# Performance work log

Measured on AMD Instinct MI355X. Metric: run time of the kernel, lower is better.

## Reference

```python
import jax, jax.numpy as jnp
import numpy as np

N_NODES = 50000
N_EDGES = 1250000
H_FEATS = 64


def setup_inputs() -> dict:
    key = jax.random.key(0)
    k1, k2, k3, k4, k5, k6, k7 = jax.random.split(key, 7)
    h = jax.random.normal(k1, (N_NODES, H_FEATS), dtype=jnp.float32)
    src = jax.random.randint(k2, (N_EDGES,), 0, N_NODES, dtype=jnp.int64)
    dst = jax.random.randint(k3, (N_EDGES,), 0, N_NODES, dtype=jnp.int64)
    # nn.Linear(2*h, h) and nn.Linear(h, 1); store weights as [in, out]
    s1 = 1.0 / np.sqrt(2 * H_FEATS)
    s2 = 1.0 / np.sqrt(H_FEATS)
    W1 = jax.random.uniform(k4, (2 * H_FEATS, H_FEATS), jnp.float32, -s1, s1)
    b1 = jax.random.uniform(k5, (H_FEATS,), jnp.float32, -s1, s1)
    W2 = jax.random.uniform(k6, (H_FEATS, 1), jnp.float32, -s2, s2)
    b2 = jax.random.uniform(k7, (1,), jnp.float32, -s2, s2)
    return {"h": h, "src": src, "dst": dst, "W1": W1, "b1": b1, "W2": W2, "b2": b2}


def reference(h, src, dst, W1, b1, W2, b2):
    # Gather per-edge endpoint features and concat: [E, 2*h_feats]
    he = jnp.concatenate([h[src], h[dst]], axis=1)
    hid = jax.nn.relu(he @ W1 + b1)          # [E, h_feats]
    score = (hid @ W2 + b2)[:, 0]            # [E]
    label = jnp.round(jax.nn.sigmoid(score))  # [E]
    return score, label
```

## Files before the change

### kernel.cpp

```cpp
#include <hip/hip_runtime.h>
#include <hip/hip_bf16.h>

#define H 64
#define NPB 64
#define EPB 128

__global__ void __launch_bounds__(256)
node_proj_kernel(const float* __restrict__ h,
                 const float* __restrict__ W1,
                 float* __restrict__ A,
                 float* __restrict__ B,
                 int n_nodes) {
    __shared__ float sh[NPB * H];
    const int t = threadIdx.x;
    const int c = t & 63;
    const int w = t >> 6;
    const int base = blockIdx.x * NPB;

    {
        const float4* hg = (const float4*)(h + (size_t)base * H);
        float4* shv = (float4*)sh;
#pragma unroll
        for (int i = 0; i < 4; ++i) {
            const int idx = t + i * 256;
            const int node = base + (idx >> 4);
            if (node < n_nodes) shv[idx] = hg[idx];
        }
    }

    float wA[64], wB[64];
#pragma unroll
    for (int k = 0; k < 64; ++k) {
        wA[k] = W1[k * H + c];
        wB[k] = W1[(k + 64) * H + c];
    }
    __syncthreads();

#pragma unroll 1
    for (int n0 = 0; n0 < 8; ++n0) {
        const int nl = w * 16 + n0 * 2;
        const int node = base + nl;
        if (node >= n_nodes) break;
        const bool two = (node + 1) < n_nodes;
        const float4* hr0 = (const float4*)(sh + nl * H);
        const float4* hr1 = (const float4*)(sh + (nl + 1) * H);
        float a0 = 0.f, b0 = 0.f, a1 = 0.f, b1acc = 0.f;
#pragma unroll
        for (int kk = 0; kk < 16; ++kk) {
            const float4 h0 = hr0[kk];
            const float4 h1 = hr1[kk];
            a0 = fmaf(h0.x, wA[4 * kk + 0], a0);
            a0 = fmaf(h0.y, wA[4 * kk + 1], a0);
            a0 = fmaf(h0.z, wA[4 * kk + 2], a0);
            a0 = fmaf(h0.w, wA[4 * kk + 3], a0);
            b0 = fmaf(h0.x, wB[4 * kk + 0], b0);
            b0 = fmaf(h0.y, wB[4 * kk + 1], b0);
            b0 = fmaf(h0.z, wB[4 * kk + 2], b0);
            b0 = fmaf(h0.w, wB[4 * kk + 3], b0);
            a1 = fmaf(h1.x, wA[4 * kk + 0], a1);
            a1 = fmaf(h1.y, wA[4 * kk + 1], a1);
            a1 = fmaf(h1.z, wA[4 * kk + 2], a1);
            a1 = fmaf(h1.w, wA[4 * kk + 3], a1);
            b1acc = fmaf(h1.x, wB[4 * kk + 0], b1acc);
            b1acc = fmaf(h1.y, wB[4 * kk + 1], b1acc);
            b1acc = fmaf(h1.z, wB[4 * kk + 2], b1acc);
            b1acc = fmaf(h1.w, wB[4 * kk + 3], b1acc);
        }
        A[(size_t)node * H + c] = a0;
        B[(size_t)node * H + c] = b0;
        if (two) {
            A[(size_t)(node + 1) * H + c] = a1;
            B[(size_t)(node + 1) * H + c] = b1acc;
        }
    }
}

__global__ void __launch_bounds__(256)
edge_score_kernel(const float* __restrict__ A,
                  const float* __restrict__ B,
                  const int* __restrict__ src,
                  const int* __restrict__ dst,
                  const float* __restrict__ b1,
                  const float* __restrict__ W2,
                  const float* __restrict__ b2,
                  float* __restrict__ score_out,
                  float* __restrict__ label_out,
                  int n_edges) {
    const int t = threadIdx.x;
    const int sub = t & 15;
    const int group = t >> 4;

    const float4 b1v = ((const float4*)b1)[sub];
    const float4 w2v = ((const float4*)W2)[sub];
    const float b2s = b2[0];

    const int e0 = blockIdx.x * EPB + group;

    int ec[8], s[8], d[8];
#pragma unroll
    for (int i = 0; i < 8; ++i) {
        const int e = e0 + i * 16;
        ec[i] = e < n_edges ? e : (n_edges - 1);
    }
#pragma unroll
    for (int i = 0; i < 8; ++i) { s[i] = src[ec[i]]; d[i] = dst[ec[i]]; }

    float4 a4[8], c4[8];
#pragma unroll
    for (int i = 0; i < 8; ++i)
        a4[i] = ((const float4*)(A + (size_t)s[i] * H))[sub];
#pragma unroll
    for (int i = 0; i < 8; ++i)
        c4[i] = ((const float4*)(B + (size_t)d[i] * H))[sub];

#pragma unroll
    for (int i = 0; i < 8; ++i) {
        const float h0 = fmaxf(a4[i].x + c4[i].x + b1v.x, 0.f);
        const float h1 = fmaxf(a4[i].y + c4[i].y + b1v.y, 0.f);
        const float h2 = fmaxf(a4[i].z + c4[i].z + b1v.z, 0.f);
        const float h3 = fmaxf(a4[i].w + c4[i].w + b1v.w, 0.f);
        float p = h0 * w2v.x + h1 * w2v.y + h2 * w2v.z + h3 * w2v.w;
        p += __shfl_xor(p, 1);
        p += __shfl_xor(p, 2);
        p += __shfl_xor(p, 4);
        p += __shfl_xor(p, 8);
        const int e = e0 + i * 16;
        if (sub == 0 && e < n_edges) {
            const float sc = p + b2s;
            score_out[e] = sc;
            label_out[e] = sc > 0.f ? 1.f : 0.f;
        }
    }
}

extern "C" void kernel_launch(void* const* d_in, const int* in_sizes, int n_in,
                              void* d_out, int out_size, void* d_ws, size_t ws_size,
                              hipStream_t stream) {
    const float* h   = (const float*)d_in[0];
    const int*   src = (const int*)  d_in[1];
    const int*   dst = (const int*)  d_in[2];
    const float* W1  = (const float*)d_in[3];
    const float* b1  = (const float*)d_in[4];
    const float* W2  = (const float*)d_in[5];
    const float* b2  = (const float*)d_in[6];

    const int n_nodes = in_sizes[0] / H;
    const int n_edges = in_sizes[1];

    float* A = (float*)d_ws;
    float* B = A + (size_t)n_nodes * H;

    float* score_out = (float*)d_out;
    float* label_out = score_out + n_edges;

    {
        const int blocks = (n_nodes + NPB - 1) / NPB;
        node_proj_kernel<<<blocks, 256, 0, stream>>>(h, W1, A, B, n_nodes);
    }
    {
        const int blocks = (n_edges + EPB - 1) / EPB;
        edge_score_kernel<<<blocks, 256, 0, stream>>>(A, B, src, dst, b1, W2, b2,
                                                      score_out, label_out, n_edges);
    }
}
```

Measured before the change: 172.7 us.

## Gather bf16 node projections in edge kernel with fp32 fallback near zero

The node projection kernel now writes both fp32 and bf16 copies of the A/B projections. The edge kernel gathers the half-size bf16 rows to cut random-gather traffic. When the resulting score is within a small threshold of zero, it re-gathers the fp32 rows and recomputes, so the label stays correct. This costs extra writes in the node kernel and a divergent fallback path, and scores away from zero carry bf16 rounding error.

After: 147.0 us. 14.9% less time.

```diff
diff --git a/kernel.cpp b/kernel.cpp
--- a/kernel.cpp
+++ b/kernel.cpp
@@ -4,12 +4,23 @@
 #define H 64
 #define NPB 64
 #define EPB 128
+#define FB_THRESH 0.015f
+
+__device__ __forceinline__ unsigned short f2bf(float f) {
+    unsigned u = __float_as_uint(f);
+    unsigned r = (u + 0x7fffu + ((u >> 16) & 1u)) >> 16;
+    return (unsigned short)r;
+}
+__device__ __forceinline__ float bf_lo(unsigned w) { return __uint_as_float(w << 16); }
+__device__ __forceinline__ float bf_hi(unsigned w) { return __uint_as_float(w & 0xffff0000u); }
 
 __global__ void __launch_bounds__(256)
 node_proj_kernel(const float* __restrict__ h,
                  const float* __restrict__ W1,
-                 float* __restrict__ A,
-                 float* __restrict__ B,
+                 float* __restrict__ A32,
+                 float* __restrict__ B32,
+                 unsigned short* __restrict__ Abf,
+                 unsigned short* __restrict__ Bbf,
                  int n_nodes) {
     __shared__ float sh[NPB * H];
     const int t = threadIdx.x;
@@ -66,18 +77,24 @@
             b1acc = fmaf(h1.z, wB[4 * kk + 2], b1acc);
             b1acc = fmaf(h1.w, wB[4 * kk + 3], b1acc);
         }
-        A[(size_t)node * H + c] = a0;
-        B[(size_t)node * H + c] = b0;
+        A32[(size_t)node * H + c] = a0;
+        B32[(size_t)node * H + c] = b0;
+        Abf[(size_t)node * H + c] = f2bf(a0);
+        Bbf[(size_t)node * H + c] = f2bf(b0);
         if (two) {
-            A[(size_t)(node + 1) * H + c] = a1;
-            B[(size_t)(node + 1) * H + c] = b1acc;
+            A32[(size_t)(node + 1) * H + c] = a1;
+            B32[(size_t)(node + 1) * H + c] = b1acc;
+            Abf[(size_t)(node + 1) * H + c] = f2bf(a1);
+            Bbf[(size_t)(node + 1) * H + c] = f2bf(b1acc);
         }
     }
 }
 
 __global__ void __launch_bounds__(256)
-edge_score_kernel(const float* __restrict__ A,
-                  const float* __restrict__ B,
+edge_score_kernel(const unsigned short* __restrict__ Abf,
+                  const unsigned short* __restrict__ Bbf,
+                  const float* __restrict__ A32,
+                  const float* __restrict__ B32,
                   const int* __restrict__ src,
                   const int* __restrict__ dst,
                   const float* __restrict__ b1,
@@ -105,28 +122,48 @@
 #pragma unroll
     for (int i = 0; i < 8; ++i) { s[i] = src[ec[i]]; d[i] = dst[ec[i]]; }
 
-    float4 a4[8], c4[8];
+    uint2 av[8], cv[8];
 #pragma unroll
     for (int i = 0; i < 8; ++i)
-        a4[i] = ((const float4*)(A + (size_t)s[i] * H))[sub];
+        av[i] = ((const uint2*)(Abf + (size_t)s[i] * H))[sub];
 #pragma unroll
     for (int i = 0; i < 8; ++i)
-        c4[i] = ((const float4*)(B + (size_t)d[i] * H))[sub];
+        cv[i] = ((const uint2*)(Bbf + (size_t)d[i] * H))[sub];
 
 #pragma unroll
     for (int i = 0; i < 8; ++i) {
-        const float h0 = fmaxf(a4[i].x + c4[i].x + b1v.x, 0.f);
-        const float h1 = fmaxf(a4[i].y + c4[i].y + b1v.y, 0.f);
-        const float h2 = fmaxf(a4[i].z + c4[i].z + b1v.z, 0.f);
-        const float h3 = fmaxf(a4[i].w + c4[i].w + b1v.w, 0.f);
+        const float a0 = bf_lo(av[i].x), a1 = bf_hi(av[i].x);
+        const float a2 = bf_lo(av[i].y), a3 = bf_hi(av[i].y);
+        const float c0 = bf_lo(cv[i].x), c1 = bf_hi(cv[i].x);
+        const float c2 = bf_lo(cv[i].y), c3 = bf_hi(cv[i].y);
+        const float h0 = fmaxf(a0 + c0 + b1v.x, 0.f);
+        const float h1 = fmaxf(a1 + c1 + b1v.y, 0.f);
+        const float h2 = fmaxf(a2 + c2 + b1v.z, 0.f);
+        const float h3 = fmaxf(a3 + c3 + b1v.w, 0.f);
         float p = h0 * w2v.x + h1 * w2v.y + h2 * w2v.z + h3 * w2v.w;
         p += __shfl_xor(p, 1);
         p += __shfl_xor(p, 2);
         p += __shfl_xor(p, 4);
         p += __shfl_xor(p, 8);
+        float sc = p + b2s;
+
+        if (fabsf(sc) < FB_THRESH) {
+            const float4 a4 = ((const float4*)(A32 + (size_t)s[i] * H))[sub];
+            const float4 c4 = ((const float4*)(B32 + (size_t)d[i] * H))[sub];
+            const float g0 = fmaxf(a4.x + c4.x + b1v.x, 0.f);
+            const float g1 = fmaxf(a4.y + c4.y + b1v.y, 0.f);
+            const float g2 = fmaxf(a4.z + c4.z + b1v.z, 0.f);
+            const float g3 = fmaxf(a4.w + c4.w + b1v.w, 0.f);
+            float q = g0 * w2v.x + g1 * w2v.y + g2 * w2v.z + g3 * w2v.w;
+            q += __shfl_xor(q, 1);
+            q += __shfl_xor(q, 2);
+            q += __shfl_xor(q, 4);
+            q += __shfl_xor(q, 8);
+            sc = q + b2s;
+        }
+
         const int e = e0 + i * 16;
         if (sub == 0 && e < n_edges) {
-            const float sc = p + b2s;
             score_out[e] = sc;
             label_out[e] = sc > 0.f ? 1.f : 0.f;
         }
@@ -147,19 +184,24 @@
     const int n_nodes = in_sizes[0] / H;
     const int n_edges = in_sizes[1];
 
-    float* A = (float*)d_ws;
-    float* B = A + (size_t)n_nodes * H;
+    float* A32 = (float*)d_ws;
+    float* B32 = A32 + (size_t)n_nodes * H;
+    unsigned short* Abf = (unsigned short*)(B32 + (size_t)n_nodes * H);
+    unsigned short* Bbf = Abf + (size_t)n_nodes * H;
 
     float* score_out = (float*)d_out;
     float* label_out = score_out + n_edges;
 
     {
         const int blocks = (n_nodes + NPB - 1) / NPB;
-        node_proj_kernel<<<blocks, 256, 0, stream>>>(h, W1, A, B, n_nodes);
+        node_proj_kernel<<<blocks, 256, 0, stream>>>(h, W1, A32, B32, Abf, Bbf,
+                                                     n_nodes);
     }
     {
         const int blocks = (n_edges + EPB - 1) / EPB;
-        edge_score_kernel<<<blocks, 256, 0, stream>>>(A, B, src, dst, b1, W2, b2,
-                                                      score_out, label_out, n_edges);
-    }
-}
+        edge_score_kernel<<<blocks, 256, 0, stream>>>(Abf, Bbf, A32, B32,
+                                                      src, dst, b1, W2, b2,
+                                                      score_out, label_out,
+                                                      n_edges);
+    }
+}
```
